# Kernel tuning notes

Hardware: AMD Instinct MI355X
Metric: run time of the kernel (lower is better)

Reference implementation:

```python
import jax, jax.numpy as jnp
import numpy as np

RADIUS = 5
WIN = (RADIUS - 1) * 2 + 1  # 9


def setup_inputs() -> dict:
    key = jax.random.key(0)
    k1, k2 = jax.random.split(key)
    B, K, H, W = 4, 4, 224, 224
    seg = jax.random.uniform(k1, (B, K, H, W), dtype=jnp.float32)
    weight = jax.random.uniform(k2, (B, 1, H, W, WIN, WIN), dtype=jnp.float32)
    return {"seg": seg, "weight": weight}


def reference(seg, weight):
    # seg: [B,K,H,W]; weight: [B,1,H,W,w,w] local affinity window, w = 2*(radius-1)+1
    B, K, H, W = seg.shape
    Kconst = jnp.float32(K)
    # torch pads by `radius` on all sides but only uses window offsets 0..2*(radius-1),
    # i.e. relative offsets [-radius, radius-2] -- replicate exactly.
    padded = jnp.pad(seg, ((0, 0), (0, 0), (RADIUS, RADIUS), (RADIUS, RADIUS)))
    # weighted sum over the local window without materializing [B,K,H,W,w,w]
    sum_w_seg = jnp.zeros_like(seg)
    for m in range(WIN):
        for n in range(WIN):
            sum_w_seg = sum_w_seg + padded[:, :, m:m + H, n:n + W] * weight[:, :, :, :, m, n]
    assocA = jnp.sum(sum_w_seg * seg, axis=(-1, -2))                      # [B,K]
    assocV = jnp.sum(jnp.sum(weight, axis=(-1, -2)) * seg, axis=(-1, -2))  # [B,K]
    assoc = jnp.sum(assocA / assocV, axis=-1)                              # [B]
    return jnp.sum(Kconst - assoc)
```

## Files before the change

kernel.cpp:

```cpp
#include <hip/hip_runtime.h>

#define RADIUS 5
#define WIN 9
#define BB 4
#define KK 4
#define HH 224
#define WW 224
#define HW (HH * WW)
#define PD 234
#define PAREA (PD * PD)
#define NBUCKET 64
#define PARTIAL_FLOATS (NBUCKET * BB * 8)
#define BLOCKS_PER_B (HW / 64)


__global__ __launch_bounds__(256) void ncuts_pad(
    const float* __restrict__ seg, float4* __restrict__ pseg)
{
    const int tid = blockIdx.x * 256 + threadIdx.x;
    if (tid >= BB * PAREA) return;
    const int b  = tid / PAREA;
    const int rc = tid - b * PAREA;
    const int r  = rc / PD;
    const int c  = rc - r * PD;
    const int hh = r - RADIUS;
    const int ww = c - RADIUS;
    float4 v = {0.f, 0.f, 0.f, 0.f};
    if (hh >= 0 && hh < HH && ww >= 0 && ww < WW) {
        const float* sb = seg + (size_t)b * KK * HW + hh * WW + ww;
        v.x = sb[0 * HW];
        v.y = sb[1 * HW];
        v.z = sb[2 * HW];
        v.w = sb[3 * HW];
    }
    pseg[tid] = v;
}

__global__ __launch_bounds__(64) void ncuts_main(
    const float* __restrict__ weight,
    const float4* __restrict__ pseg,
    float* __restrict__ partial)
{
    __shared__ float wlds[64 * 81];

    const int lane = threadIdx.x;
    const int tid  = blockIdx.x * 64 + lane;
    const int b    = tid / HW;
    const int rem  = tid - b * HW;
    const int h    = rem / WW;
    const int w    = rem - h * WW;

    const float4* wsrc = (const float4*)(weight + (size_t)blockIdx.x * (64 * 81));
    float4* wdst = (float4*)wlds;
    #pragma unroll
    for (int j = 0; j < 20; ++j)
        wdst[j * 64 + lane] = wsrc[j * 64 + lane];
    if (lane < 16)
        wdst[1280 + lane] = wsrc[1280 + lane];
    __syncthreads();

    const float4* p4 = pseg + (size_t)b * PAREA;
    const float* wl  = &wlds[lane * 81];

    float a0 = 0.f, a1 = 0.f, a2 = 0.f, a3 = 0.f, wsum = 0.f;

    #pragma unroll
    for (int m = 0; m < WIN; ++m) {
        const int base = (h + m) * PD + w;
        #pragma unroll
        for (int n = 0; n < WIN; ++n) {
            const float wv = wl[m * WIN + n];
            const float4 s = p4[base + n];
            a0 = fmaf(wv, s.x, a0);
            a1 = fmaf(wv, s.y, a1);
            a2 = fmaf(wv, s.z, a2);
            a3 = fmaf(wv, s.w, a3);
            wsum += wv;
        }
    }

    const float4 t = p4[(h + RADIUS) * PD + (w + RADIUS)];

    float vals[8] = { a0 * t.x, a1 * t.y, a2 * t.z, a3 * t.w,
                      wsum * t.x, wsum * t.y, wsum * t.z, wsum * t.w };

    #pragma unroll
    for (int i = 0; i < 8; ++i) {
        float v = vals[i];
        v += __shfl_down(v, 32);
        v += __shfl_down(v, 16);
        v += __shfl_down(v, 8);
        v += __shfl_down(v, 4);
        v += __shfl_down(v, 2);
        v += __shfl_down(v, 1);
        vals[i] = v;
    }

    if (lane == 0) {
        const int bb     = blockIdx.x - b * BLOCKS_PER_B;
        const int bucket = bb & (NBUCKET - 1);
        float* dst = partial + (bucket * BB + b) * 8;
        #pragma unroll
        for (int i = 0; i < 8; ++i)
            atomicAdd(dst + i, vals[i]);
    }
}

__global__ __launch_bounds__(64) void ncuts_final(
    const float* __restrict__ partial, float* __restrict__ out)
{
    __shared__ float sums[32];
    const int t = threadIdx.x;
    if (t < 32) {
        const int b = t >> 3;
        const int i = t & 7;
        float s = 0.f;
        for (int bucket = 0; bucket < NBUCKET; ++bucket)
            s += partial[(bucket * BB + b) * 8 + i];
        sums[b * 8 + i] = s;
    }
    __syncthreads();
    if (t == 0) {
        float total = 0.f;
        for (int b = 0; b < BB; ++b) {
            float assoc = 0.f;
            for (int k = 0; k < KK; ++k) {
                const float A = sums[b * 8 + k];
                const float V = sums[b * 8 + 4 + k];
                assoc += A / V;
            }
            total += (float)KK - assoc;
        }
        out[0] = total;
    }
}

extern "C" void kernel_launch(void* const* d_in, const int* in_sizes, int n_in,
                              void* d_out, int out_size, void* d_ws, size_t ws_size,
                              hipStream_t stream) {
    const float* seg    = (const float*)d_in[0];
    const float* weight = (const float*)d_in[1];
    float* out     = (float*)d_out;
    float* wsf     = (float*)d_ws;
    float* partial = wsf;
    float4* pseg   = (float4*)(wsf + PARTIAL_FLOATS);

    hipMemsetAsync(d_ws, 0, PARTIAL_FLOATS * sizeof(float), stream);

    {
        const int total = BB * PAREA;
        const int grid  = (total + 255) / 256;
        hipLaunchKernelGGL(ncuts_pad, dim3(grid), dim3(256), 0, stream, seg, pseg);
    }

    {
        const int grid = BB * BLOCKS_PER_B;
        hipLaunchKernelGGL(ncuts_main, dim3(grid), dim3(64), 0, stream,
                           weight, pseg, partial);
    }

    hipLaunchKernelGGL(ncuts_final, dim3(1), dim3(64), 0, stream, partial, out);
}
```

Baseline: 106.7 us.

## Stream weight taps directly with coalesced per-tap indexing instead of LDS staging

```diff
diff --git a/kernel.cpp b/kernel.cpp
--- a/kernel.cpp
+++ b/kernel.cpp
@@ -11,7 +11,8 @@
 #define PAREA (PD * PD)
 #define NBUCKET 64
 #define PARTIAL_FLOATS (NBUCKET * BB * 8)
-#define BLOCKS_PER_B (HW / 64)
+#define WAVES_PER_B (HW / 64)
+#define ELEMS_PER_WAVE (64 * 81)
 
 
 __global__ __launch_bounds__(256) void ncuts_pad(
@@ -36,53 +37,58 @@
     pseg[tid] = v;
 }
 
-__global__ __launch_bounds__(64) void ncuts_main(
+__global__ __launch_bounds__(256, 4) void ncuts_main(
     const float* __restrict__ weight,
     const float4* __restrict__ pseg,
     float* __restrict__ partial)
 {
-    __shared__ float wlds[64 * 81];
+    const int lane = threadIdx.x & 63;
+    const int wid  = blockIdx.x * 4 + (threadIdx.x >> 6);
+    const int b    = wid / WAVES_PER_B;
 
-    const int lane = threadIdx.x;
-    const int tid  = blockIdx.x * 64 + lane;
-    const int b    = tid / HW;
-    const int rem  = tid - b * HW;
-    const int h    = rem / WW;
-    const int w    = rem - h * WW;
+    const float* wbase = weight + (size_t)wid * ELEMS_PER_WAVE;
+    const float4* p4   = pseg + (size_t)b * PAREA;
 
-    const float4* wsrc = (const float4*)(weight + (size_t)blockIdx.x * (64 * 81));
-    float4* wdst = (float4*)wlds;
-    #pragma unroll
-    for (int j = 0; j < 20; ++j)
-        wdst[j * 64 + lane] = wsrc[j * 64 + lane];
-    if (lane < 16)
-        wdst[1280 + lane] = wsrc[1280 + lane];
-    __syncthreads();
+    const int pix0 = wid * 64;
+    const int rem0 = pix0 - b * HW;
+    int h = rem0 / WW;
+    int w = rem0 - h * WW;
+    int rowoff = h * PD + w;
+    int tap = lane;
 
-    const float4* p4 = pseg + (size_t)b * PAREA;
-    const float* wl  = &wlds[lane * 81];
+    float a0 = 0.f, a1 = 0.f, a2 = 0.f, a3 = 0.f;
+    float v0 = 0.f, v1 = 0.f, v2 = 0.f, v3 = 0.f;
 
-    float a0 = 0.f, a1 = 0.f, a2 = 0.f, a3 = 0.f, wsum = 0.f;
+    #pragma unroll 3
+    for (int t = 0; t < 81; ++t) {
+        const float wv = wbase[t * 64 + lane];
 
-    #pragma unroll
-    for (int m = 0; m < WIN; ++m) {
-        const int base = (h + m) * PD + w;
-        #pragma unroll
-        for (int n = 0; n < WIN; ++n) {
-            const float wv = wl[m * WIN + n];
-            const float4 s = p4[base + n];
-            a0 = fmaf(wv, s.x, a0);
-            a1 = fmaf(wv, s.y, a1);
-            a2 = fmaf(wv, s.z, a2);
-            a3 = fmaf(wv, s.w, a3);
-            wsum += wv;
+        const int m = (tap * 57) >> 9;
+        const int n = tap - 9 * m;
+
+        const float4 s = p4[rowoff + m * PD + n];
+        const float4 o = p4[rowoff + (RADIUS * PD + RADIUS)];
+
+        a0 = fmaf(wv * s.x, o.x, a0);
+        a1 = fmaf(wv * s.y, o.y, a1);
+        a2 = fmaf(wv * s.z, o.z, a2);
+        a3 = fmaf(wv * s.w, o.w, a3);
+        v0 = fmaf(wv, o.x, v0);
+        v1 = fmaf(wv, o.y, v1);
+        v2 = fmaf(wv, o.z, v2);
+        v3 = fmaf(wv, o.w, v3);
+
+        const int t2 = tap + 64;
+        const bool wrap = (t2 >= 81);
+        tap = wrap ? t2 - 81 : t2;
+        if (wrap) {
+            const bool roww = (w == WW - 1);
+            w = roww ? 0 : w + 1;
+            rowoff += roww ? (PD - WW + 1) : 1;
         }
     }
 
-    const float4 t = p4[(h + RADIUS) * PD + (w + RADIUS)];
-
-    float vals[8] = { a0 * t.x, a1 * t.y, a2 * t.z, a3 * t.w,
-                      wsum * t.x, wsum * t.y, wsum * t.z, wsum * t.w };
+    float vals[8] = { a0, a1, a2, a3, v0, v1, v2, v3 };
 
     #pragma unroll
     for (int i = 0; i < 8; ++i) {
@@ -97,8 +103,7 @@
     }
 
     if (lane == 0) {
-        const int bb     = blockIdx.x - b * BLOCKS_PER_B;
-        const int bucket = bb & (NBUCKET - 1);
+        const int bucket = wid & (NBUCKET - 1);
         float* dst = partial + (bucket * BB + b) * 8;
         #pragma unroll
         for (int i = 0; i < 8; ++i)
@@ -152,12 +157,10 @@
         const int grid  = (total + 255) / 256;
         hipLaunchKernelGGL(ncuts_pad, dim3(grid), dim3(256), 0, stream, seg, pseg);
     }
-
     {
-        const int grid = BB * BLOCKS_PER_B;
-        hipLaunchKernelGGL(ncuts_main, dim3(grid), dim3(64), 0, stream,
+        const int grid = (BB * WAVES_PER_B) / 4;
+        hipLaunchKernelGGL(ncuts_main, dim3(grid), dim3(256), 0, stream,
                            weight, pseg, partial);
     }
-
     hipLaunchKernelGGL(ncuts_final, dim3(1), dim3(64), 0, stream, partial, out);
 }
```

Measured after the change: 125.0 us. 1.17x slower.

## Split the 81-tap window across four wavefronts per 64-pixel block

Applied to the files above, without the earlier changes.

```diff
diff --git a/kernel.cpp b/kernel.cpp
--- a/kernel.cpp
+++ b/kernel.cpp
@@ -11,7 +11,10 @@
 #define PAREA (PD * PD)
 #define NBUCKET 64
 #define PARTIAL_FLOATS (NBUCKET * BB * 8)
-#define BLOCKS_PER_B (HW / 64)
+
+#define PX_PER_BLOCK 64
+#define BLOCKS_TOTAL (BB * HW / PX_PER_BLOCK)
+#define WF4_PER_BLOCK (PX_PER_BLOCK * 81 / 4)
 
 
 __global__ __launch_bounds__(256) void ncuts_pad(
@@ -36,53 +39,69 @@
     pseg[tid] = v;
 }
 
-__global__ __launch_bounds__(64) void ncuts_main(
-    const float* __restrict__ weight,
+template<int T0, int T1>
+__device__ __forceinline__ void do_taps(const float* __restrict__ wl,
+                                        const float4* __restrict__ pb, int roff,
+                                        float& a0, float& a1, float& a2, float& a3,
+                                        float& wsum)
+{
+    #pragma unroll
+    for (int tap = T0; tap < T1; ++tap) {
+        const int m = tap / 9;
+        const int n = tap - 9 * m;
+        const float wv = wl[tap];
+        const float4 s = pb[roff + m * PD + n];
+        a0 = fmaf(wv, s.x, a0);
+        a1 = fmaf(wv, s.y, a1);
+        a2 = fmaf(wv, s.z, a2);
+        a3 = fmaf(wv, s.w, a3);
+        wsum += wv;
+    }
+}
+
+__global__ __launch_bounds__(256, 7) void ncuts_main(
+    const float4* __restrict__ weight4,
     const float4* __restrict__ pseg,
     float* __restrict__ partial)
 {
-    __shared__ float wlds[64 * 81];
+    __shared__ float wlds[PX_PER_BLOCK * 81];
 
-    const int lane = threadIdx.x;
-    const int tid  = blockIdx.x * 64 + lane;
-    const int b    = tid / HW;
-    const int rem  = tid - b * HW;
-    const int h    = rem / WW;
-    const int w    = rem - h * WW;
+    const int tid  = threadIdx.x;
+    const int lane = tid & 63;
+    const int ws   = tid >> 6;
 
-    const float4* wsrc = (const float4*)(weight + (size_t)blockIdx.x * (64 * 81));
+    const float4* wsrc = weight4 + (size_t)blockIdx.x * WF4_PER_BLOCK;
     float4* wdst = (float4*)wlds;
     #pragma unroll
-    for (int j = 0; j < 20; ++j)
-        wdst[j * 64 + lane] = wsrc[j * 64 + lane];
-    if (lane < 16)
-        wdst[1280 + lane] = wsrc[1280 + lane];
+    for (int it = 0; it < 6; ++it) {
+        const int idx = it * 256 + tid;
+        if (idx < WF4_PER_BLOCK) wdst[idx] = wsrc[idx];
+    }
     __syncthreads();
 
-    const float4* p4 = pseg + (size_t)b * PAREA;
+    const int px  = blockIdx.x * PX_PER_BLOCK + lane;
+    const int b   = px / HW;
+    const int rem = px - b * HW;
+    const int h   = rem / WW;
+    const int w   = rem - h * WW;
+    const int roff = h * PD + w;
+
+    const float4* pb = pseg + (size_t)b * PAREA;
     const float* wl  = &wlds[lane * 81];
 
     float a0 = 0.f, a1 = 0.f, a2 = 0.f, a3 = 0.f, wsum = 0.f;
 
-    #pragma unroll
-    for (int m = 0; m < WIN; ++m) {
-        const int base = (h + m) * PD + w;
-        #pragma unroll
-        for (int n = 0; n < WIN; ++n) {
-            const float wv = wl[m * WIN + n];
-            const float4 s = p4[base + n];
-            a0 = fmaf(wv, s.x, a0);
-            a1 = fmaf(wv, s.y, a1);
-            a2 = fmaf(wv, s.z, a2);
-            a3 = fmaf(wv, s.w, a3);
-            wsum += wv;
-        }
+    switch (ws) {
+        case 0: do_taps< 0, 21>(wl, pb, roff, a0, a1, a2, a3, wsum); break;
+        case 1: do_taps<21, 41>(wl, pb, roff, a0, a1, a2, a3, wsum); break;
+        case 2: do_taps<41, 61>(wl, pb, roff, a0, a1, a2, a3, wsum); break;
+        default: do_taps<61, 81>(wl, pb, roff, a0, a1, a2, a3, wsum); break;
     }
 
-    const float4 t = p4[(h + RADIUS) * PD + (w + RADIUS)];
+    const float4 o = pb[roff + RADIUS * PD + RADIUS];
 
-    float vals[8] = { a0 * t.x, a1 * t.y, a2 * t.z, a3 * t.w,
-                      wsum * t.x, wsum * t.y, wsum * t.z, wsum * t.w };
+    float vals[8] = { a0 * o.x, a1 * o.y, a2 * o.z, a3 * o.w,
+                      wsum * o.x, wsum * o.y, wsum * o.z, wsum * o.w };
 
     #pragma unroll
     for (int i = 0; i < 8; ++i) {
@@ -97,8 +116,7 @@
     }
 
     if (lane == 0) {
-        const int bb     = blockIdx.x - b * BLOCKS_PER_B;
-        const int bucket = bb & (NBUCKET - 1);
+        const int bucket = (blockIdx.x * 4 + ws) & (NBUCKET - 1);
         float* dst = partial + (bucket * BB + b) * 8;
         #pragma unroll
         for (int i = 0; i < 8; ++i)
@@ -138,8 +156,8 @@
 extern "C" void kernel_launch(void* const* d_in, const int* in_sizes, int n_in,
                               void* d_out, int out_size, void* d_ws, size_t ws_size,
                               hipStream_t stream) {
-    const float* seg    = (const float*)d_in[0];
-    const float* weight = (const float*)d_in[1];
+    const float* seg     = (const float*)d_in[0];
+    const float4* weight = (const float4*)d_in[1];
     float* out     = (float*)d_out;
     float* wsf     = (float*)d_ws;
     float* partial = wsf;
@@ -152,12 +170,9 @@
         const int grid  = (total + 255) / 256;
         hipLaunchKernelGGL(ncuts_pad, dim3(grid), dim3(256), 0, stream, seg, pseg);
     }
-
     {
-        const int grid = BB * BLOCKS_PER_B;
-        hipLaunchKernelGGL(ncuts_main, dim3(grid), dim3(64), 0, stream,
+        hipLaunchKernelGGL(ncuts_main, dim3(BLOCKS_TOTAL), dim3(256), 0, stream,
                            weight, pseg, partial);
     }
-
     hipLaunchKernelGGL(ncuts_final, dim3(1), dim3(64), 0, stream, partial, out);
 }
```

After: 123.0 us. +15.3%, slower.
